# Kernel tuning notes

Measured on AMD Instinct MI355X. Metric: run time of the kernel, lower is better.

The kernel has to match this reference:

```python
import jax, jax.numpy as jnp
import numpy as np

B, N, D = 8, 2048, 256

def setup_inputs() -> dict:
    key = jax.random.key(0)
    k1, k2, k3, k4 = jax.random.split(key, 4)
    x1 = jax.random.normal(k1, (B, N, D), dtype=jnp.float32)
    x2 = jax.random.normal(k2, (B, N, D), dtype=jnp.float32)
    W = jax.random.normal(k3, (D, D), dtype=jnp.float32) * (1.0 / np.sqrt(D))
    b = jax.random.normal(k4, (D,), dtype=jnp.float32) * 0.01
    return {"x1": x1, "x2": x2, "W": W, "b": b}

def reference(x1, x2, W, b):
    # torch Linear: q = x1 @ W^T + b
    q = jnp.einsum('bnd,ed->bne', x1, W) + b            # [B, N1, D]
    scores = jnp.einsum('bnd,bmd->bnm', q, x2)          # [B, N1, N2]
    scores = jax.nn.softmax(scores, axis=-1)
    x1_updated = jnp.einsum('bnm,bmd->bnd', scores, x2)  # [B, N1, D]
    x2_updated = jnp.einsum('bnm,bnd->bmd', scores, x1)  # scores^T @ x1 -> [B, N2, D]
    return (x1_updated, x2_updated)
```

## Files before the change

kernel.cpp:

```cpp
#include <hip/hip_runtime.h>

#define BB 8
#define NN 2048
#define DD 256

typedef unsigned short u16;
typedef float f32x4 __attribute__((ext_vector_type(4)));
typedef short s16x8 __attribute__((ext_vector_type(8)));
typedef __bf16 bf16x8 __attribute__((ext_vector_type(8)));
typedef _Float16 f16x8 __attribute__((ext_vector_type(8)));
typedef unsigned short u16x4 __attribute__((ext_vector_type(4)));

#define MFMA_BF(a, b, c)                                                       \
  __builtin_amdgcn_mfma_f32_16x16x32_bf16(__builtin_bit_cast(bf16x8, (a)),     \
                                          __builtin_bit_cast(bf16x8, (b)),     \
                                          (c), 0, 0, 0)
#define MFMA_F16(a, b, c)                                                      \
  __builtin_amdgcn_mfma_f32_16x16x32_f16(__builtin_bit_cast(f16x8, (a)),       \
                                         __builtin_bit_cast(f16x8, (b)),       \
                                         (c), 0, 0, 0)

__device__ inline u16 f2bf(float f) {
  union { float f; unsigned u; } v; v.f = f;
  unsigned r = v.u + 0x7FFFu + ((v.u >> 16) & 1u);
  return (u16)(r >> 16);
}
__device__ inline float bf2f(u16 h) {
  union { unsigned u; float f; } v; v.u = ((unsigned)h) << 16;
  return v.f;
}
__device__ inline u16 f2h(float f) {
  _Float16 h = (_Float16)f;
  return __builtin_bit_cast(unsigned short, h);
}
__device__ inline float h2f(u16 h) {
  _Float16 x = __builtin_bit_cast(_Float16, h);
  return (float)x;
}
struct HL { short h, l; };
__device__ inline HL splitbf(float f) {
  HL r;
  u16 hh = f2bf(f);
  r.h = (short)hh;
  r.l = (short)f2bf(f - bf2f(hh));
  return r;
}
__device__ inline void split8(const f32x4 a, const f32x4 c, s16x8& h, s16x8& lo) {
#pragma unroll
  for (int i = 0; i < 4; ++i) {
    HL r = splitbf(a[i]);
    h[i] = r.h; lo[i] = r.l;
  }
#pragma unroll
  for (int i = 0; i < 4; ++i) {
    HL r = splitbf(c[i]);
    h[4 + i] = r.h; lo[4 + i] = r.l;
  }
}
__device__ inline s16x8 cvt8h(const f32x4 a, const f32x4 c) {
  s16x8 h;
#pragma unroll
  for (int i = 0; i < 4; ++i) h[i] = (short)f2h(a[i]);
#pragma unroll
  for (int i = 0; i < 4; ++i) h[4 + i] = (short)f2h(c[i]);
  return h;
}

__global__ __launch_bounds__(256) void k_conv2(const float* __restrict__ x1,
                                               const float* __restrict__ x2,
                                               u16* __restrict__ xb1T,
                                               u16* __restrict__ xb2T) {
  __shared__ u16 t[64][68];
  const int zz = blockIdx.z;
  const float* src = (zz < 8) ? x1 : x2;
  u16* dstT = (zz < 8) ? xb1T : xb2T;
  const int b = zz & 7;
  const int n0 = blockIdx.x * 64;
  const int d0 = blockIdx.y * 64;
  const int tid = threadIdx.x;
  const int r = tid >> 4;
  const int c4 = tid & 15;
#pragma unroll
  for (int rr = 0; rr < 4; ++rr) {
    const int row = r + rr * 16;
    const float4 v = *(const float4*)&src[(size_t)(b * NN + n0 + row) * DD + d0 + c4 * 4];
    u16x4 o2 = {f2h(v.x), f2h(v.y), f2h(v.z), f2h(v.w)};
    *(u16x4*)&t[row][c4 * 4] = o2;
  }
  __syncthreads();
  const int d = tid >> 2;
  const int ch = tid & 3;
  u16 buf[16];
#pragma unroll
  for (int j = 0; j < 16; ++j) buf[j] = t[ch * 16 + j][d];
  u16* outp = &dstT[(size_t)(b * DD + d0 + d) * NN + n0 + ch * 16];
  s16x8 v0, v1;
#pragma unroll
  for (int j = 0; j < 8; ++j) { v0[j] = (short)buf[j]; v1[j] = (short)buf[8 + j]; }
  *(s16x8*)outp = v0;
  *(s16x8*)(outp + 8) = v1;
}

__global__ __launch_bounds__(256) void k_qgemm(const float* __restrict__ x1,
                                               const float* __restrict__ W,
                                               const float* __restrict__ bias,
                                               u16* __restrict__ qf) {
  __shared__ char wl[131072];
  const int tid = threadIdx.x;
  const int w = tid >> 6, l = tid & 63, lr = l & 15, lg = l >> 4;
  const int row0 = blockIdx.x * 64 + w * 16;

  s16x8 afh[8], afl[8];
#pragma unroll
  for (int ks = 0; ks < 8; ++ks) {
    const f32x4 a = *(const f32x4*)&x1[(size_t)(row0 + lr) * DD + ks * 32 + lg * 8];
    const f32x4 c = *(const f32x4*)&x1[(size_t)(row0 + lr) * DD + ks * 32 + lg * 8 + 4];
    split8(a, c, afh[ks], afl[ks]);
  }

  const f32x4 zero4 = {0.f, 0.f, 0.f, 0.f};
  f32x4 acc[16];
#pragma unroll
  for (int i = 0; i < 16; ++i) acc[i] = zero4;

  const int er = tid >> 1;
  const int kh = tid & 1;

  for (int eh = 0; eh < 2; ++eh) {
    __syncthreads();
    {
      const int e = eh * 128 + er;
#pragma unroll
      for (int j = 0; j < 16; ++j) {
        const f32x4 a = *(const f32x4*)&W[(size_t)e * DD + kh * 128 + j * 8];
        const f32x4 c = *(const f32x4*)&W[(size_t)e * DD + kh * 128 + j * 8 + 4];
        s16x8 h, lo;
        split8(a, c, h, lo);
        int off = er * 512 + kh * 256 + j * 16;
        off ^= (er & 7) << 4;
        *(s16x8*)(wl + off) = h;
        *(s16x8*)(wl + 65536 + off) = lo;
      }
    }
    __syncthreads();
#pragma unroll
    for (int ct = 0; ct < 8; ++ct) {
      const int el = ct * 16 + lr;
#pragma unroll
      for (int ks = 0; ks < 8; ++ks) {
        int off = el * 512 + ks * 64 + lg * 16;
        off ^= (el & 7) << 4;
        const s16x8 bh = *(const s16x8*)(wl + off);
        const s16x8 bl = *(const s16x8*)(wl + 65536 + off);
        f32x4 acv = acc[eh * 8 + ct];
        acv = MFMA_BF(afh[ks], bh, acv);
        acv = MFMA_BF(afl[ks], bh, acv);
        acv = MFMA_BF(afh[ks], bl, acv);
        acc[eh * 8 + ct] = acv;
      }
    }
  }

#pragma unroll
  for (int i = 0; i < 16; ++i) {
    const int col = (i >> 3) * 128 + (i & 7) * 16 + lr;
    const float bb = bias[col];
#pragma unroll
    for (int r = 0; r < 4; ++r) {
      const int orow = row0 + lg * 4 + r;
      qf[(size_t)orow * DD + col] = f2h(acc[i][r] + bb);
    }
  }
}

__global__ __launch_bounds__(256, 2) void k_flashB(const u16* __restrict__ qf_g,
                                                   const float* __restrict__ x2f,
                                                   const u16* __restrict__ xb2T,
                                                   u16* __restrict__ opart,
                                                   float2* __restrict__ ml) {
  __shared__ char smem[69632];
  const int tid = threadIdx.x;
  const int w = tid >> 6, l = tid & 63, lr = l & 15, lg = l >> 4;
  const int bid = blockIdx.x;
  const int b = bid & 7, nt = (bid >> 3) & 31, g = bid >> 8;
  const int n0 = nt * 64;

  s16x8 qfr[8];
  {
    const size_t qoff = (size_t)(b * NN + n0 + w * 16 + lr) * DD;
#pragma unroll
    for (int ks = 0; ks < 8; ++ks)
      qfr[ks] = *(const s16x8*)(qf_g + qoff + ks * 32 + lg * 8);
  }

  const f32x4 zero4 = {0.f, 0.f, 0.f, 0.f};
  f32x4 o[16];
#pragma unroll
  for (int i = 0; i < 16; ++i) o[i] = zero4;
  float M[4] = {-INFINITY, -INFINITY, -INFINITY, -INFINITY};
  float L[4] = {0.f, 0.f, 0.f, 0.f};

  const float* srcF = x2f + (size_t)b * NN * DD;
  const char* srcT = (const char*)(xb2T + (size_t)b * DD * NN);
  char* plds = smem + 65536 + w * 1024;

  const int r2 = tid >> 4;
  const int c2 = tid & 15;
  const int sdT = tid;

  f32x4 ff[8];
  s16x8 stT[4];
  auto LOADS = [&](int m0) {
#pragma unroll
    for (int h = 0; h < 2; ++h)
#pragma unroll
      for (int j = 0; j < 4; ++j)
        ff[h * 4 + j] = *(const f32x4*)&srcF[(size_t)(m0 + r2 + h * 16) * DD + c2 * 16 + j * 4];
#pragma unroll
    for (int q = 0; q < 4; ++q)
      stT[q] = *(const s16x8*)(srcT + (size_t)sdT * 4096 + (size_t)m0 * 2 + q * 16);
  };
  auto WRITES = [&](int buf) {
    char* bN = smem + buf * 32768;
    char* bT = bN + 16384;
#pragma unroll
    for (int h = 0; h < 2; ++h) {
      const int row = r2 + h * 16;
#pragma unroll
      for (int p = 0; p < 2; ++p) {
        const s16x8 hh = cvt8h(ff[h * 4 + p * 2], ff[h * 4 + p * 2 + 1]);
        int off = row * 512 + c2 * 32 + p * 16;
        off ^= (row & 7) << 4;
        *(s16x8*)(bN + off) = hh;
      }
    }
#pragma unroll
    for (int q = 0; q < 4; ++q) {
      int off = sdT * 64 + q * 16;
      off ^= (sdT & 7) << 4;
      *(s16x8*)(bT + off) = stT[q];
    }
  };

  LOADS(g * 1024);
  WRITES(0);
  LOADS(g * 1024 + 32);
  __syncthreads();

  for (int t = 0; t < 32; ++t) {
    const int cur = t & 1;
    if (t < 31) WRITES(cur ^ 1);
    if (t < 30) LOADS(g * 1024 + (t + 2) * 32);
    const char* bN = smem + cur * 32768;
    const char* bT = bN + 16384;

    f32x4 s0 = zero4, s1 = zero4;
#pragma unroll
    for (int ks = 0; ks < 8; ++ks) {
      int off0 = (lr * 512 + ks * 64 + lg * 16) ^ ((lr & 7) << 4);
      const s16x8 b0 = *(const s16x8*)(bN + off0);
      s0 = MFMA_F16(qfr[ks], b0, s0);
      const int m1 = 16 + lr;
      int off1 = (m1 * 512 + ks * 64 + lg * 16) ^ ((m1 & 7) << 4);
      const s16x8 b1 = *(const s16x8*)(bN + off1);
      s1 = MFMA_F16(qfr[ks], b1, s1);
    }

    float p0[4], p1[4];
#pragma unroll
    for (int r = 0; r < 4; ++r) {
      float tm = fmaxf(s0[r], s1[r]);
      tm = fmaxf(tm, __shfl_xor(tm, 1));
      tm = fmaxf(tm, __shfl_xor(tm, 2));
      tm = fmaxf(tm, __shfl_xor(tm, 4));
      tm = fmaxf(tm, __shfl_xor(tm, 8));
      const float Mn = fmaxf(M[r], tm);
      const float corr = __expf(M[r] - Mn);
      M[r] = Mn;
      p0[r] = __expf(s0[r] - Mn);
      p1[r] = __expf(s1[r] - Mn);
      L[r] = L[r] * corr + p0[r] + p1[r];
#pragma unroll
      for (int dt = 0; dt < 16; ++dt) o[dt][r] *= corr;
    }

#pragma unroll
    for (int r = 0; r < 4; ++r) {
      const int row = lg * 4 + r;
      const int key = (row & 7) << 4;
      int o0 = (row * 64 + lr * 2) ^ key;
      int o1 = (row * 64 + 32 + lr * 2) ^ key;
      *(u16*)(plds + o0) = f2h(p0[r]);
      *(u16*)(plds + o1) = f2h(p1[r]);
    }
    int ra = (lr * 64 + lg * 16) ^ ((lr & 7) << 4);
    const s16x8 pa = *(const s16x8*)(plds + ra);

#pragma unroll
    for (int dt = 0; dt < 16; ++dt) {
      const int dl = dt * 16 + lr;
      int off = (dl * 64 + lg * 16) ^ ((dl & 7) << 4);
      const s16x8 bv = *(const s16x8*)(bT + off);
      o[dt] = MFMA_F16(pa, bv, o[dt]);
    }

    __syncthreads();
  }

#pragma unroll
  for (int r = 0; r < 4; ++r) {
    float s = L[r];
    s += __shfl_xor(s, 1); s += __shfl_xor(s, 2);
    s += __shfl_xor(s, 4); s += __shfl_xor(s, 8);
    L[r] = s;
  }

  const int blin = b * 32 + nt;
  u16* pb = opart + (((size_t)(g * 1024 + blin * 4 + w)) << 12);
#pragma unroll
  for (int dt = 0; dt < 16; ++dt) {
    u16x4 v = {f2h(o[dt][0]), f2h(o[dt][1]), f2h(o[dt][2]), f2h(o[dt][3])};
    *(u16x4*)(pb + ((dt * 64 + l) << 2)) = v;
  }
  if (lr == 0) {
#pragma unroll
    for (int r = 0; r < 4; ++r) {
      float2 v = {M[r], L[r]};
      ml[g * 16384 + b * 2048 + n0 + w * 16 + lg * 4 + r] = v;
    }
  }
}

__global__ __launch_bounds__(256) void k_mergeB(const u16* __restrict__ opart,
                                                const float2* __restrict__ ml,
                                                float* __restrict__ out0,
                                                float* __restrict__ lse) {
  __shared__ float4 cf[16];
  const int bid = blockIdx.x;
  const int blin = bid >> 2, wg = bid & 3;
  const int b = blin >> 5, nt = blin & 31;
  const int tid = threadIdx.x;
  const int row0 = b * 2048 + nt * 64 + wg * 16;
  if (tid < 16) {
    const float2 m0 = ml[row0 + tid];
    const float2 m1 = ml[16384 + row0 + tid];
    const float Mf = fmaxf(m0.x, m1.x);
    const float c0 = __expf(m0.x - Mf);
    const float c1 = __expf(m1.x - Mf);
    const float Lf = m0.y * c0 + m1.y * c1;
    float4 v = {c0, c1, 1.f / Lf, 0.f};
    cf[tid] = v;
    lse[row0 + tid] = Mf + __logf(Lf);
  }
  __syncthreads();
  const int lane = tid & 63;
  const size_t base0 = ((size_t)(blin * 4 + wg)) << 12;
  const size_t base1 = base0 + (1024ull << 12);
#pragma unroll
  for (int k = 0; k < 4; ++k) {
    const int dt = (tid >> 6) * 4 + k;
    const u16x4 v0 = *(const u16x4*)(opart + base0 + ((dt * 64 + lane) << 2));
    const u16x4 v1 = *(const u16x4*)(opart + base1 + ((dt * 64 + lane) << 2));
#pragma unroll
    for (int r = 0; r < 4; ++r) {
      const int i = (lane >> 4) * 4 + r;
      const float4 c = cf[i];
      const float val = (h2f((u16)v0[r]) * c.x + h2f((u16)v1[r]) * c.y) * c.z;
      out0[(size_t)(row0 + i) * DD + dt * 16 + (lane & 15)] = val;
    }
  }
}

__global__ __launch_bounds__(256, 2) void k_passC(const float* __restrict__ x2f,
                                                  const u16* __restrict__ qf_g,
                                                  const u16* __restrict__ xb1T,
                                                  const float* __restrict__ lse,
                                                  u16* __restrict__ opart) {
  __shared__ char smem[69632];
  const int tid = threadIdx.x;
  const int w = tid >> 6, l = tid & 63, lr = l & 15, lg = l >> 4;
  const int bid = blockIdx.x;
  const int b = bid & 7, mt = (bid >> 3) & 31, g = bid >> 8;
  const int m0 = mt * 64;

  s16x8 xf[8];
  {
    const float* xp = x2f + (size_t)(b * NN + m0 + w * 16 + lr) * DD;
#pragma unroll
    for (int ks = 0; ks < 8; ++ks) {
      const f32x4 a = *(const f32x4*)(xp + ks * 32 + lg * 8);
      const f32x4 c = *(const f32x4*)(xp + ks * 32 + lg * 8 + 4);
      xf[ks] = cvt8h(a, c);
    }
  }

  const f32x4 zero4 = {0.f, 0.f, 0.f, 0.f};
  f32x4 o[16];
#pragma unroll
  for (int i = 0; i < 16; ++i) o[i] = zero4;

  const char* srcQ = (const char*)(qf_g + (size_t)b * NN * DD);
  const char* srcT = (const char*)(xb1T + (size_t)b * DD * NN);
  const float* lsb = lse + (size_t)b * NN;
  char* plds = smem + 65536 + w * 1024;

  const int smN = tid >> 3;
  const int sjN = tid & 7;
  const int sdT = tid;

  s16x8 stQ[4], stT[4];
  auto LOADS = [&](int nn0) {
#pragma unroll
    for (int q = 0; q < 4; ++q) {
      stQ[q] = *(const s16x8*)(srcQ + (size_t)(nn0 + smN) * 512 + sjN * 64 + q * 16);
      stT[q] = *(const s16x8*)(srcT + (size_t)sdT * 4096 + (size_t)nn0 * 2 + q * 16);
    }
  };
  auto WRITES = [&](int buf) {
    char* bQ = smem + buf * 32768;
    char* bT = bQ + 16384;
#pragma unroll
    for (int q = 0; q < 4; ++q) {
      int off = smN * 512 + sjN * 64 + q * 16;
      off ^= (smN & 7) << 4;
      *(s16x8*)(bQ + off) = stQ[q];
      int offT = sdT * 64 + q * 16;
      offT ^= (sdT & 7) << 4;
      *(s16x8*)(bT + offT) = stT[q];
    }
  };

  LOADS(g * 1024);
  WRITES(0);
  LOADS(g * 1024 + 32);
  __syncthreads();

  for (int t = 0; t < 32; ++t) {
    const int cur = t & 1;
    if (t < 31) WRITES(cur ^ 1);
    if (t < 30) LOADS(g * 1024 + (t + 2) * 32);
    const char* bQ = smem + cur * 32768;
    const char* bT = bQ + 16384;

    f32x4 s0 = zero4, s1 = zero4;
#pragma unroll
    for (int ks = 0; ks < 8; ++ks) {
      int off0 = (lr * 512 + ks * 64 + lg * 16) ^ ((lr & 7) << 4);
      const s16x8 b0 = *(const s16x8*)(bQ + off0);
      s0 = MFMA_F16(xf[ks], b0, s0);
      const int n1 = 16 + lr;
      int off1 = (n1 * 512 + ks * 64 + lg * 16) ^ ((n1 & 7) << 4);
      const s16x8 b1 = *(const s16x8*)(bQ + off1);
      s1 = MFMA_F16(xf[ks], b1, s1);
    }

    const int nb = g * 1024 + t * 32;
    const float lv0 = lsb[nb + lr];
    const float lv1 = lsb[nb + 16 + lr];
    float p0[4], p1[4];
#pragma unroll
    for (int r = 0; r < 4; ++r) {
      p0[r] = __expf(s0[r] - lv0);
      p1[r] = __expf(s1[r] - lv1);
    }

#pragma unroll
    for (int r = 0; r < 4; ++r) {
      const int row = lg * 4 + r;
      const int key = (row & 7) << 4;
      int o0 = (row * 64 + lr * 2) ^ key;
      int o1 = (row * 64 + 32 + lr * 2) ^ key;
      *(u16*)(plds + o0) = f2h(p0[r]);
      *(u16*)(plds + o1) = f2h(p1[r]);
    }
    int ra = (lr * 64 + lg * 16) ^ ((lr & 7) << 4);
    const s16x8 pa = *(const s16x8*)(plds + ra);

#pragma unroll
    for (int dt = 0; dt < 16; ++dt) {
      const int dl = dt * 16 + lr;
      int off = (dl * 64 + lg * 16) ^ ((dl & 7) << 4);
      const s16x8 bv = *(const s16x8*)(bT + off);
      o[dt] = MFMA_F16(pa, bv, o[dt]);
    }

    __syncthreads();
  }

  const int blin = b * 32 + mt;
  u16* pb = opart + (((size_t)(g * 1024 + blin * 4 + w)) << 12);
#pragma unroll
  for (int dt = 0; dt < 16; ++dt) {
    u16x4 v = {f2h(o[dt][0]), f2h(o[dt][1]), f2h(o[dt][2]), f2h(o[dt][3])};
    *(u16x4*)(pb + ((dt * 64 + l) << 2)) = v;
  }
}

__global__ __launch_bounds__(256) void k_mergeC(const u16* __restrict__ opart,
                                                float* __restrict__ out1) {
  const int bid = blockIdx.x;
  const int blin = bid >> 2, wg = bid & 3;
  const int b = blin >> 5, mt = blin & 31;
  const int tid = threadIdx.x;
  const int row0 = b * 2048 + mt * 64 + wg * 16;
  const int lane = tid & 63;
  const size_t base0 = ((size_t)(blin * 4 + wg)) << 12;
  const size_t base1 = base0 + (1024ull << 12);
#pragma unroll
  for (int k = 0; k < 4; ++k) {
    const int dt = (tid >> 6) * 4 + k;
    const u16x4 v0 = *(const u16x4*)(opart + base0 + ((dt * 64 + lane) << 2));
    const u16x4 v1 = *(const u16x4*)(opart + base1 + ((dt * 64 + lane) << 2));
#pragma unroll
    for (int r = 0; r < 4; ++r) {
      const int i = (lane >> 4) * 4 + r;
      out1[(size_t)(row0 + i) * DD + dt * 16 + (lane & 15)] =
          h2f((u16)v0[r]) + h2f((u16)v1[r]);
    }
  }
}

extern "C" void kernel_launch(void* const* d_in, const int* in_sizes, int n_in,
                              void* d_out, int out_size, void* d_ws, size_t ws_size,
                              hipStream_t stream) {
  (void)in_sizes; (void)n_in; (void)out_size; (void)ws_size;
  const float* x1 = (const float*)d_in[0];
  const float* x2 = (const float*)d_in[1];
  const float* W  = (const float*)d_in[2];
  const float* bs = (const float*)d_in[3];
  float* out0 = (float*)d_out;
  float* out1 = out0 + (size_t)BB * NN * DD;

  char* ws = (char*)d_ws;
  u16* xb2T   = (u16*)(ws);
  u16* xb1T   = (u16*)(ws + 8388608);
  float2* ml  = (float2*)(ws + 16777216);
  float* lseb = (float*)(ws + 17039360);
  u16* opart  = (u16*)(ws + 17104896);
  u16* qf = (u16*)out1;

  k_conv2<<<dim3(32, 4, 16), 256, 0, stream>>>(x1, x2, xb1T, xb2T);
  k_qgemm<<<256, 256, 0, stream>>>(x1, W, bs, qf);
  k_flashB<<<512, 256, 0, stream>>>(qf, x2, xb2T, opart, ml);
  k_mergeB<<<1024, 256, 0, stream>>>(opart, ml, out0, lseb);
  k_passC<<<512, 256, 0, stream>>>(x2, qf, xb1T, lseb, opart);
  k_mergeC<<<1024, 256, 0, stream>>>(opart, out1);
}
```

Baseline: 211.3 us.

## Split D output dimension across wave pairs in flash and passC kernels

```diff
diff --git a/kernel.cpp b/kernel.cpp
--- a/kernel.cpp
+++ b/kernel.cpp
@@ -173,30 +173,31 @@
   }
 }
 
-__global__ __launch_bounds__(256, 2) void k_flashB(const u16* __restrict__ qf_g,
+__global__ __launch_bounds__(512, 4) void k_flashB(const u16* __restrict__ qf_g,
                                                    const float* __restrict__ x2f,
                                                    const u16* __restrict__ xb2T,
                                                    u16* __restrict__ opart,
                                                    float2* __restrict__ ml) {
-  __shared__ char smem[69632];
+  __shared__ char smem[73728];
   const int tid = threadIdx.x;
   const int w = tid >> 6, l = tid & 63, lr = l & 15, lg = l >> 4;
+  const int nw = w >> 1, dh = w & 1;
   const int bid = blockIdx.x;
   const int b = bid & 7, nt = (bid >> 3) & 31, g = bid >> 8;
   const int n0 = nt * 64;
 
   s16x8 qfr[8];
   {
-    const size_t qoff = (size_t)(b * NN + n0 + w * 16 + lr) * DD;
+    const size_t qoff = (size_t)(b * NN + n0 + nw * 16 + lr) * DD;
 #pragma unroll
     for (int ks = 0; ks < 8; ++ks)
       qfr[ks] = *(const s16x8*)(qf_g + qoff + ks * 32 + lg * 8);
   }
 
   const f32x4 zero4 = {0.f, 0.f, 0.f, 0.f};
-  f32x4 o[16];
-#pragma unroll
-  for (int i = 0; i < 16; ++i) o[i] = zero4;
+  f32x4 o[8];
+#pragma unroll
+  for (int i = 0; i < 8; ++i) o[i] = zero4;
   float M[4] = {-INFINITY, -INFINITY, -INFINITY, -INFINITY};
   float L[4] = {0.f, 0.f, 0.f, 0.f};
 
@@ -204,42 +205,33 @@
   const char* srcT = (const char*)(xb2T + (size_t)b * DD * NN);
   char* plds = smem + 65536 + w * 1024;
 
-  const int r2 = tid >> 4;
-  const int c2 = tid & 15;
-  const int sdT = tid;
-
-  f32x4 ff[8];
-  s16x8 stT[4];
+  const int rN = tid >> 4;
+  const int cN = tid & 15;
+  const int drT = tid >> 1;
+  const int hfT = tid & 1;
+
+  f32x4 ff[4];
+  s16x8 stT[2];
   auto LOADS = [&](int m0) {
 #pragma unroll
-    for (int h = 0; h < 2; ++h)
-#pragma unroll
-      for (int j = 0; j < 4; ++j)
-        ff[h * 4 + j] = *(const f32x4*)&srcF[(size_t)(m0 + r2 + h * 16) * DD + c2 * 16 + j * 4];
-#pragma unroll
-    for (int q = 0; q < 4; ++q)
-      stT[q] = *(const s16x8*)(srcT + (size_t)sdT * 4096 + (size_t)m0 * 2 + q * 16);
+    for (int j = 0; j < 4; ++j)
+      ff[j] = *(const f32x4*)&srcF[(size_t)(m0 + rN) * DD + cN * 16 + j * 4];
+#pragma unroll
+    for (int j = 0; j < 2; ++j)
+      stT[j] = *(const s16x8*)(srcT + (size_t)drT * 4096 + (size_t)m0 * 2 + hfT * 32 + j * 16);
   };
   auto WRITES = [&](int buf) {
-    char* bN = smem + buf * 32768;
-    char* bT = bN + 16384;
-#pragma unroll
-    for (int h = 0; h < 2; ++h) {
-      const int row = r2 + h * 16;
-#pragma unroll
-      for (int p = 0; p < 2; ++p) {
-        const s16x8 hh = cvt8h(ff[h * 4 + p * 2], ff[h * 4 + p * 2 + 1]);
-        int off = row * 512 + c2 * 32 + p * 16;
-        off ^= (row & 7) << 4;
-        *(s16x8*)(bN + off) = hh;
-      }
-    }
-#pragma unroll
-    for (int q = 0; q < 4; ++q) {
-      int off = sdT * 64 + q * 16;
-      off ^= (sdT & 7) << 4;
-      *(s16x8*)(bT + off) = stT[q];
-    }
+    char* bN = smem + buf * 16384;
+    char* bT = smem + 32768 + buf * 16384;
+    const int keyN = (rN & 7) << 4;
+    const s16x8 h0 = cvt8h(ff[0], ff[1]);
+    const s16x8 h1 = cvt8h(ff[2], ff[3]);
+    *(s16x8*)(bN + ((rN * 512 + cN * 32) ^ keyN)) = h0;
+    *(s16x8*)(bN + ((rN * 512 + cN * 32 + 16) ^ keyN)) = h1;
+    const int keyT = (drT & 7) << 4;
+#pragma unroll
+    for (int j = 0; j < 2; ++j)
+      *(s16x8*)(bT + ((drT * 64 + hfT * 32 + j * 16) ^ keyT)) = stT[j];
   };
 
   LOADS(g * 1024);
@@ -251,8 +243,8 @@
     const int cur = t & 1;
     if (t < 31) WRITES(cur ^ 1);
     if (t < 30) LOADS(g * 1024 + (t + 2) * 32);
-    const char* bN = smem + cur * 32768;
-    const char* bT = bN + 16384;
+    const char* bN = smem + cur * 16384;
+    const char* bT = smem + 32768 + cur * 16384;
 
     f32x4 s0 = zero4, s1 = zero4;
 #pragma unroll
@@ -281,7 +273,7 @@
       p1[r] = __expf(s1[r] - Mn);
       L[r] = L[r] * corr + p0[r] + p1[r];
 #pragma unroll
-      for (int dt = 0; dt < 16; ++dt) o[dt][r] *= corr;
+      for (int dt = 0; dt < 8; ++dt) o[dt][r] *= corr;
     }
 
 #pragma unroll
@@ -297,8 +289,8 @@
     const s16x8 pa = *(const s16x8*)(plds + ra);
 
 #pragma unroll
-    for (int dt = 0; dt < 16; ++dt) {
-      const int dl = dt * 16 + lr;
+    for (int dt = 0; dt < 8; ++dt) {
+      const int dl = dh * 128 + dt * 16 + lr;
       int off = (dl * 64 + lg * 16) ^ ((dl & 7) << 4);
       const s16x8 bv = *(const s16x8*)(bT + off);
       o[dt] = MFMA_F16(pa, bv, o[dt]);
@@ -316,17 +308,17 @@
   }
 
   const int blin = b * 32 + nt;
-  u16* pb = opart + (((size_t)(g * 1024 + blin * 4 + w)) << 12);
-#pragma unroll
-  for (int dt = 0; dt < 16; ++dt) {
+  u16* pb = opart + (((size_t)((g * 256 + blin) * 8 + w)) << 11);
+#pragma unroll
+  for (int dt = 0; dt < 8; ++dt) {
     u16x4 v = {f2h(o[dt][0]), f2h(o[dt][1]), f2h(o[dt][2]), f2h(o[dt][3])};
     *(u16x4*)(pb + ((dt * 64 + l) << 2)) = v;
   }
-  if (lr == 0) {
+  if (dh == 0 && lr == 0) {
 #pragma unroll
     for (int r = 0; r < 4; ++r) {
       float2 v = {M[r], L[r]};
-      ml[g * 16384 + b * 2048 + n0 + w * 16 + lg * 4 + r] = v;
+      ml[g * 16384 + b * 2048 + n0 + nw * 16 + lg * 4 + r] = v;
     }
   }
 }
@@ -337,10 +329,9 @@
                                                 float* __restrict__ lse) {
   __shared__ float4 cf[16];
   const int bid = blockIdx.x;
-  const int blin = bid >> 2, wg = bid & 3;
-  const int b = blin >> 5, nt = blin & 31;
+  const int blin = bid >> 2, nw = bid & 3;
   const int tid = threadIdx.x;
-  const int row0 = b * 2048 + nt * 64 + wg * 16;
+  const int row0 = (blin >> 5) * 2048 + (blin & 31) * 64 + nw * 16;
   if (tid < 16) {
     const float2 m0 = ml[row0 + tid];
     const float2 m1 = ml[16384 + row0 + tid];
@@ -354,38 +345,40 @@
   }
   __syncthreads();
   const int lane = tid & 63;
-  const size_t base0 = ((size_t)(blin * 4 + wg)) << 12;
-  const size_t base1 = base0 + (1024ull << 12);
 #pragma unroll
   for (int k = 0; k < 4; ++k) {
-    const int dt = (tid >> 6) * 4 + k;
-    const u16x4 v0 = *(const u16x4*)(opart + base0 + ((dt * 64 + lane) << 2));
-    const u16x4 v1 = *(const u16x4*)(opart + base1 + ((dt * 64 + lane) << 2));
+    const int dd = (tid >> 6) * 4 + k;
+    const int dh = dd >> 3, dt = dd & 7;
+    const size_t c0b = ((size_t)((0 * 256 + blin) * 8 + nw * 2 + dh)) << 11;
+    const size_t c1b = ((size_t)((1 * 256 + blin) * 8 + nw * 2 + dh)) << 11;
+    const u16x4 v0 = *(const u16x4*)(opart + c0b + ((dt * 64 + lane) << 2));
+    const u16x4 v1 = *(const u16x4*)(opart + c1b + ((dt * 64 + lane) << 2));
 #pragma unroll
     for (int r = 0; r < 4; ++r) {
       const int i = (lane >> 4) * 4 + r;
       const float4 c = cf[i];
-      const float val = (h2f((u16)v0[r]) * c.x + h2f((u16)v1[r]) * c.y) * c.z;
-      out0[(size_t)(row0 + i) * DD + dt * 16 + (lane & 15)] = val;
-    }
-  }
-}
-
-__global__ __launch_bounds__(256, 2) void k_passC(const float* __restrict__ x2f,
+      out0[(size_t)(row0 + i) * DD + dh * 128 + dt * 16 + (lane & 15)] =
+          (h2f((u16)v0[r]) * c.x + h2f((u16)v1[r]) * c.y) * c.z;
+    }
+  }
+}
+
+__global__ __launch_bounds__(512, 4) void k_passC(const float* __restrict__ x2f,
                                                   const u16* __restrict__ qf_g,
                                                   const u16* __restrict__ xb1T,
                                                   const float* __restrict__ lse,
                                                   u16* __restrict__ opart) {
-  __shared__ char smem[69632];
+  __shared__ char smem[73728];
   const int tid = threadIdx.x;
   const int w = tid >> 6, l = tid & 63, lr = l & 15, lg = l >> 4;
+  const int nw = w >> 1, dh = w & 1;
   const int bid = blockIdx.x;
   const int b = bid & 7, mt = (bid >> 3) & 31, g = bid >> 8;
   const int m0 = mt * 64;
 
   s16x8 xf[8];
   {
-    const float* xp = x2f + (size_t)(b * NN + m0 + w * 16 + lr) * DD;
+    const float* xp = x2f + (size_t)(b * NN + m0 + nw * 16 + lr) * DD;
 #pragma unroll
     for (int ks = 0; ks < 8; ++ks) {
       const f32x4 a = *(const f32x4*)(xp + ks * 32 + lg * 8);
@@ -395,38 +388,37 @@
   }
 
   const f32x4 zero4 = {0.f, 0.f, 0.f, 0.f};
-  f32x4 o[16];
-#pragma unroll
-  for (int i = 0; i < 16; ++i) o[i] = zero4;
+  f32x4 o[8];
+#pragma unroll
+  for (int i = 0; i < 8; ++i) o[i] = zero4;
 
   const char* srcQ = (const char*)(qf_g + (size_t)b * NN * DD);
   const char* srcT = (const char*)(xb1T + (size_t)b * DD * NN);
   const float* lsb = lse + (size_t)b * NN;
   char* plds = smem + 65536 + w * 1024;
 
-  const int smN = tid >> 3;
-  const int sjN = tid & 7;
-  const int sdT = tid;
-
-  s16x8 stQ[4], stT[4];
+  const int rN = tid >> 4;
+  const int cN = tid & 15;
+  const int drT = tid >> 1;
+  const int hfT = tid & 1;
+
+  s16x8 stQ[2], stT[2];
   auto LOADS = [&](int nn0) {
 #pragma unroll
-    for (int q = 0; q < 4; ++q) {
-      stQ[q] = *(const s16x8*)(srcQ + (size_t)(nn0 + smN) * 512 + sjN * 64 + q * 16);
-      stT[q] = *(const s16x8*)(srcT + (size_t)sdT * 4096 + (size_t)nn0 * 2 + q * 16);
+    for (int j = 0; j < 2; ++j) {
+      stQ[j] = *(const s16x8*)(srcQ + (size_t)(nn0 + rN) * 512 + cN * 32 + j * 16);
+      stT[j] = *(const s16x8*)(srcT + (size_t)drT * 4096 + (size_t)nn0 * 2 + hfT * 32 + j * 16);
     }
   };
   auto WRITES = [&](int buf) {
-    char* bQ = smem + buf * 32768;
-    char* bT = bQ + 16384;
-#pragma unroll
-    for (int q = 0; q < 4; ++q) {
-      int off = smN * 512 + sjN * 64 + q * 16;
-      off ^= (smN & 7) << 4;
-      *(s16x8*)(bQ + off) = stQ[q];
-      int offT = sdT * 64 + q * 16;
-      offT ^= (sdT & 7) << 4;
-      *(s16x8*)(bT + offT) = stT[q];
+    char* bQ = smem + buf * 16384;
+    char* bT = smem + 32768 + buf * 16384;
+    const int keyQ = (rN & 7) << 4;
+    const int keyT = (drT & 7) << 4;
+#pragma unroll
+    for (int j = 0; j < 2; ++j) {
+      *(s16x8*)(bQ + ((rN * 512 + cN * 32 + j * 16) ^ keyQ)) = stQ[j];
+      *(s16x8*)(bT + ((drT * 64 + hfT * 32 + j * 16) ^ keyT)) = stT[j];
     }
   };
 
@@ -439,8 +431,8 @@
     const int cur = t & 1;
     if (t < 31) WRITES(cur ^ 1);
     if (t < 30) LOADS(g * 1024 + (t + 2) * 32);
-    const char* bQ = smem + cur * 32768;
-    const char* bT = bQ + 16384;
+    const char* bQ = smem + cur * 16384;
+    const char* bT = smem + 32768 + cur * 16384;
 
     f32x4 s0 = zero4, s1 = zero4;
 #pragma unroll
@@ -477,8 +469,8 @@
     const s16x8 pa = *(const s16x8*)(plds + ra);
 
 #pragma unroll
-    for (int dt = 0; dt < 16; ++dt) {
-      const int dl = dt * 16 + lr;
+    for (int dt = 0; dt < 8; ++dt) {
+      const int dl = dh * 128 + dt * 16 + lr;
       int off = (dl * 64 + lg * 16) ^ ((dl & 7) << 4);
       const s16x8 bv = *(const s16x8*)(bT + off);
       o[dt] = MFMA_F16(pa, bv, o[dt]);
@@ -488,9 +480,9 @@
   }
 
   const int blin = b * 32 + mt;
-  u16* pb = opart + (((size_t)(g * 1024 + blin * 4 + w)) << 12);
-#pragma unroll
-  for (int dt = 0; dt < 16; ++dt) {
+  u16* pb = opart + (((size_t)((g * 256 + blin) * 8 + w)) << 11);
+#pragma unroll
+  for (int dt = 0; dt < 8; ++dt) {
     u16x4 v = {f2h(o[dt][0]), f2h(o[dt][1]), f2h(o[dt][2]), f2h(o[dt][3])};
     *(u16x4*)(pb + ((dt * 64 + l) << 2)) = v;
   }
@@ -499,22 +491,22 @@
 __global__ __launch_bounds__(256) void k_mergeC(const u16* __restrict__ opart,
                                                 float* __restrict__ out1) {
   const int bid = blockIdx.x;
-  const int blin = bid >> 2, wg = bid & 3;
-  const int b = blin >> 5, mt = blin & 31;
+  const int blin = bid >> 2, nw = bid & 3;
   const int tid = threadIdx.x;
-  const int row0 = b * 2048 + mt * 64 + wg * 16;
+  const int row0 = (blin >> 5) * 2048 + (blin & 31) * 64 + nw * 16;
   const int lane = tid & 63;
-  const size_t base0 = ((size_t)(blin * 4 + wg)) << 12;
-  const size_t base1 = base0 + (1024ull << 12);
 #pragma unroll
   for (int k = 0; k < 4; ++k) {
-    const int dt = (tid >> 6) * 4 + k;
-    const u16x4 v0 = *(const u16x4*)(opart + base0 + ((dt * 64 + lane) << 2));
-    const u16x4 v1 = *(const u16x4*)(opart + base1 + ((dt * 64 + lane) << 2));
+    const int dd = (tid >> 6) * 4 + k;
+    const int dh = dd >> 3, dt = dd & 7;
+    const size_t c0b = ((size_t)((0 * 256 + blin) * 8 + nw * 2 + dh)) << 11;
+    const size_t c1b = ((size_t)((1 * 256 + blin) * 8 + nw * 2 + dh)) << 11;
+    const u16x4 v0 = *(const u16x4*)(opart + c0b + ((dt * 64 + lane) << 2));
+    const u16x4 v1 = *(const u16x4*)(opart + c1b + ((dt * 64 + lane) << 2));
 #pragma unroll
     for (int r = 0; r < 4; ++r) {
       const int i = (lane >> 4) * 4 + r;
-      out1[(size_t)(row0 + i) * DD + dt * 16 + (lane & 15)] =
+      out1[(size_t)(row0 + i) * DD + dh * 128 + dt * 16 + (lane & 15)] =
           h2f((u16)v0[r]) + h2f((u16)v1[r]);
     }
   }
@@ -532,17 +524,17 @@
   float* out1 = out0 + (size_t)BB * NN * DD;
 
   char* ws = (char*)d_ws;
-  u16* xb2T   = (u16*)(ws);
-  u16* xb1T   = (u16*)(ws + 8388608);
-  float2* ml  = (float2*)(ws + 16777216);
-  float* lseb = (float*)(ws + 17039360);
-  u16* opart  = (u16*)(ws + 17104896);
-  u16* qf = (u16*)out1;
+  u16* xb2T  = (u16*)(ws);
+  u16* xb1T  = (u16*)(ws + 8388608);
+  u16* opart = (u16*)(ws + 16777216);
+  u16* qf     = (u16*)out1;
+  float2* ml  = (float2*)((char*)out1 + 8388608);
+  float* lseb = (float*)((char*)out1 + 8650752);
 
   k_conv2<<<dim3(32, 4, 16), 256, 0, stream>>>(x1, x2, xb1T, xb2T);
   k_qgemm<<<256, 256, 0, stream>>>(x1, W, bs, qf);
-  k_flashB<<<512, 256, 0, stream>>>(qf, x2, xb2T, opart, ml);
+  k_flashB<<<512, 512, 0, stream>>>(qf, x2, xb2T, opart, ml);
   k_mergeB<<<1024, 256, 0, stream>>>(opart, ml, out0, lseb);
-  k_passC<<<512, 256, 0, stream>>>(x2, qf, xb1T, lseb, opart);
+  k_passC<<<512, 512, 0, stream>>>(x2, qf, xb1T, lseb, opart);
   k_mergeC<<<1024, 256, 0, stream>>>(opart, out1);
 }
```

New measurement: 295.3 us. 1.4x slower.

## Stage flash tiles via global_load_lds and pre-convert x2 to fp16

Applied to the files above, without the earlier changes.

```diff
diff --git a/kernel.cpp b/kernel.cpp
--- a/kernel.cpp
+++ b/kernel.cpp
@@ -66,14 +66,22 @@
   return h;
 }
 
+__device__ inline void gll16(const void* g, void* l) {
+  __builtin_amdgcn_global_load_lds(
+      (const __attribute__((address_space(1))) unsigned int*)g,
+      (__attribute__((address_space(3))) unsigned int*)l, 16, 0, 0);
+}
+
 __global__ __launch_bounds__(256) void k_conv2(const float* __restrict__ x1,
                                                const float* __restrict__ x2,
                                                u16* __restrict__ xb1T,
-                                               u16* __restrict__ xb2T) {
+                                               u16* __restrict__ xb2T,
+                                               u16* __restrict__ xb2n) {
   __shared__ u16 t[64][68];
   const int zz = blockIdx.z;
   const float* src = (zz < 8) ? x1 : x2;
   u16* dstT = (zz < 8) ? xb1T : xb2T;
+  u16* dstN = (zz < 8) ? (u16*)0 : xb2n;
   const int b = zz & 7;
   const int n0 = blockIdx.x * 64;
   const int d0 = blockIdx.y * 64;
@@ -85,6 +93,8 @@
     const int row = r + rr * 16;
     const float4 v = *(const float4*)&src[(size_t)(b * NN + n0 + row) * DD + d0 + c4 * 4];
     u16x4 o2 = {f2h(v.x), f2h(v.y), f2h(v.z), f2h(v.w)};
+    if (dstN)
+      *(u16x4*)&dstN[(size_t)(b * NN + n0 + row) * DD + d0 + c4 * 4] = o2;
     *(u16x4*)&t[row][c4 * 4] = o2;
   }
   __syncthreads();
@@ -174,7 +184,7 @@
 }
 
 __global__ __launch_bounds__(256, 2) void k_flashB(const u16* __restrict__ qf_g,
-                                                   const float* __restrict__ x2f,
+                                                   const u16* __restrict__ xb2n,
                                                    const u16* __restrict__ xb2T,
                                                    u16* __restrict__ opart,
                                                    float2* __restrict__ ml) {
@@ -200,57 +210,40 @@
   float M[4] = {-INFINITY, -INFINITY, -INFINITY, -INFINITY};
   float L[4] = {0.f, 0.f, 0.f, 0.f};
 
-  const float* srcF = x2f + (size_t)b * NN * DD;
-  const char* srcT = (const char*)(xb2T + (size_t)b * DD * NN);
+  const u16* xnb = xb2n + (size_t)b * NN * DD;
+  const u16* xtb = xb2T + (size_t)b * DD * NN;
   char* plds = smem + 65536 + w * 1024;
 
-  const int r2 = tid >> 4;
-  const int c2 = tid & 15;
-  const int sdT = tid;
-
-  f32x4 ff[8];
-  s16x8 stT[4];
-  auto LOADS = [&](int m0) {
-#pragma unroll
-    for (int h = 0; h < 2; ++h)
-#pragma unroll
-      for (int j = 0; j < 4; ++j)
-        ff[h * 4 + j] = *(const f32x4*)&srcF[(size_t)(m0 + r2 + h * 16) * DD + c2 * 16 + j * 4];
-#pragma unroll
-    for (int q = 0; q < 4; ++q)
-      stT[q] = *(const s16x8*)(srcT + (size_t)sdT * 4096 + (size_t)m0 * 2 + q * 16);
-  };
-  auto WRITES = [&](int buf) {
+  const u16* srcN[4];
+  const u16* srcT[4];
+#pragma unroll
+  for (int j = 0; j < 4; ++j) {
+    const int idx = j * 4096 + w * 1024 + l * 16;
+    const int rowN = idx >> 9;
+    const int colN = ((idx & 511) ^ ((rowN & 7) << 4)) >> 1;
+    srcN[j] = xnb + (size_t)rowN * DD + colN;
+    const int da = (idx >> 6) ^ ((idx >> 8) & 1);
+    const int sA = idx ^ ((da & 7) << 4);
+    srcT[j] = xtb + (size_t)(sA >> 6) * NN + ((sA & 63) >> 1);
+  }
+
+  auto ISSUE = [&](int buf, int m0) {
     char* bN = smem + buf * 32768;
     char* bT = bN + 16384;
 #pragma unroll
-    for (int h = 0; h < 2; ++h) {
-      const int row = r2 + h * 16;
-#pragma unroll
-      for (int p = 0; p < 2; ++p) {
-        const s16x8 hh = cvt8h(ff[h * 4 + p * 2], ff[h * 4 + p * 2 + 1]);
-        int off = row * 512 + c2 * 32 + p * 16;
-        off ^= (row & 7) << 4;
-        *(s16x8*)(bN + off) = hh;
-      }
-    }
-#pragma unroll
-    for (int q = 0; q < 4; ++q) {
-      int off = sdT * 64 + q * 16;
-      off ^= (sdT & 7) << 4;
-      *(s16x8*)(bT + off) = stT[q];
-    }
+    for (int j = 0; j < 4; ++j)
+      gll16(srcN[j] + (size_t)m0 * DD, bN + j * 4096 + w * 1024);
+#pragma unroll
+    for (int j = 0; j < 4; ++j)
+      gll16(srcT[j] + m0, bT + j * 4096 + w * 1024);
   };
 
-  LOADS(g * 1024);
-  WRITES(0);
-  LOADS(g * 1024 + 32);
+  ISSUE(0, g * 1024);
   __syncthreads();
 
   for (int t = 0; t < 32; ++t) {
     const int cur = t & 1;
-    if (t < 31) WRITES(cur ^ 1);
-    if (t < 30) LOADS(g * 1024 + (t + 2) * 32);
+    if (t < 31) ISSUE(cur ^ 1, g * 1024 + (t + 1) * 32);
     const char* bN = smem + cur * 32768;
     const char* bT = bN + 16384;
 
@@ -399,46 +392,41 @@
 #pragma unroll
   for (int i = 0; i < 16; ++i) o[i] = zero4;
 
-  const char* srcQ = (const char*)(qf_g + (size_t)b * NN * DD);
-  const char* srcT = (const char*)(xb1T + (size_t)b * DD * NN);
+  const u16* qfb = qf_g + (size_t)b * NN * DD;
+  const u16* xtb = xb1T + (size_t)b * DD * NN;
   const float* lsb = lse + (size_t)b * NN;
   char* plds = smem + 65536 + w * 1024;
 
-  const int smN = tid >> 3;
-  const int sjN = tid & 7;
-  const int sdT = tid;
-
-  s16x8 stQ[4], stT[4];
-  auto LOADS = [&](int nn0) {
-#pragma unroll
-    for (int q = 0; q < 4; ++q) {
-      stQ[q] = *(const s16x8*)(srcQ + (size_t)(nn0 + smN) * 512 + sjN * 64 + q * 16);
-      stT[q] = *(const s16x8*)(srcT + (size_t)sdT * 4096 + (size_t)nn0 * 2 + q * 16);
-    }
-  };
-  auto WRITES = [&](int buf) {
+  const u16* srcQ[4];
+  const u16* srcT[4];
+#pragma unroll
+  for (int j = 0; j < 4; ++j) {
+    const int idx = j * 4096 + w * 1024 + l * 16;
+    const int rowN = idx >> 9;
+    const int colN = ((idx & 511) ^ ((rowN & 7) << 4)) >> 1;
+    srcQ[j] = qfb + (size_t)rowN * DD + colN;
+    const int da = (idx >> 6) ^ ((idx >> 8) & 1);
+    const int sA = idx ^ ((da & 7) << 4);
+    srcT[j] = xtb + (size_t)(sA >> 6) * NN + ((sA & 63) >> 1);
+  }
+
+  auto ISSUE = [&](int buf, int nn0) {
     char* bQ = smem + buf * 32768;
     char* bT = bQ + 16384;
 #pragma unroll
-    for (int q = 0; q < 4; ++q) {
-      int off = smN * 512 + sjN * 64 + q * 16;
-      off ^= (smN & 7) << 4;
-      *(s16x8*)(bQ + off) = stQ[q];
-      int offT = sdT * 64 + q * 16;
-      offT ^= (sdT & 7) << 4;
-      *(s16x8*)(bT + offT) = stT[q];
-    }
+    for (int j = 0; j < 4; ++j)
+      gll16(srcQ[j] + (size_t)nn0 * DD, bQ + j * 4096 + w * 1024);
+#pragma unroll
+    for (int j = 0; j < 4; ++j)
+      gll16(srcT[j] + nn0, bT + j * 4096 + w * 1024);
   };
 
-  LOADS(g * 1024);
-  WRITES(0);
-  LOADS(g * 1024 + 32);
+  ISSUE(0, g * 1024);
   __syncthreads();
 
   for (int t = 0; t < 32; ++t) {
     const int cur = t & 1;
-    if (t < 31) WRITES(cur ^ 1);
-    if (t < 30) LOADS(g * 1024 + (t + 2) * 32);
+    if (t < 31) ISSUE(cur ^ 1, g * 1024 + (t + 1) * 32);
     const char* bQ = smem + cur * 32768;
     const char* bT = bQ + 16384;
 
@@ -532,16 +520,17 @@
   float* out1 = out0 + (size_t)BB * NN * DD;
 
   char* ws = (char*)d_ws;
-  u16* xb2T   = (u16*)(ws);
-  u16* xb1T   = (u16*)(ws + 8388608);
-  float2* ml  = (float2*)(ws + 16777216);
-  float* lseb = (float*)(ws + 17039360);
-  u16* opart  = (u16*)(ws + 17104896);
-  u16* qf = (u16*)out1;
-
-  k_conv2<<<dim3(32, 4, 16), 256, 0, stream>>>(x1, x2, xb1T, xb2T);
+  u16* xb2T  = (u16*)(ws);
+  u16* xb1T  = (u16*)(ws + 8388608);
+  u16* opart = (u16*)(ws + 16777216);
+  u16* xb2n   = (u16*)out0;
+  u16* qf     = (u16*)out1;
+  float2* ml  = (float2*)((char*)out1 + 8388608);
+  float* lseb = (float*)((char*)out1 + 8650752);
+
+  k_conv2<<<dim3(32, 4, 16), 256, 0, stream>>>(x1, x2, xb1T, xb2T, xb2n);
   k_qgemm<<<256, 256, 0, stream>>>(x1, W, bs, qf);
-  k_flashB<<<512, 256, 0, stream>>>(qf, x2, xb2T, opart, ml);
+  k_flashB<<<512, 256, 0, stream>>>(qf, xb2n, xb2T, opart, ml);
   k_mergeB<<<1024, 256, 0, stream>>>(opart, ml, out0, lseb);
   k_passC<<<512, 256, 0, stream>>>(x2, qf, xb1T, lseb, opart);
   k_mergeC<<<1024, 256, 0, stream>>>(opart, out1);
```

Measured after the change: 183.5 us. -13.2%, faster.
